# Performance work log

Hardware: AMD Instinct MI355X
Metric: run time of the kernel (lower is better)

The kernel has to match this reference:

```python
import jax, jax.numpy as jnp
import numpy as np

WINDOW = 5
MAX_LEVELS = 4
EPS = 1e-6

_SX = (jnp.array([[-1., 0., 1.], [-2., 0., 2.], [-1., 0., 1.]], dtype=jnp.float32) / 8.0).reshape(1, 1, 3, 3)
_SY = jnp.transpose(_SX, (0, 1, 3, 2))
_DN = ('NCHW', 'OIHW', 'NCHW')


def _avg_pool2(x):
    B, C, H, W = x.shape
    return x.reshape(B, C, H // 2, 2, W // 2, 2).mean(axis=(3, 5))


def _warp(img, flow):
    # bilinear grid_sample, align_corners=True, zeros padding; sample at pixel coords grid+flow
    B, C, H, W = img.shape
    ys, xs = jnp.meshgrid(jnp.arange(H, dtype=img.dtype), jnp.arange(W, dtype=img.dtype), indexing='ij')
    x = xs[None] + flow[:, 0]  # [B,H,W]
    y = ys[None] + flow[:, 1]
    x0f, y0f = jnp.floor(x), jnp.floor(y)
    wx, wy = x - x0f, y - y0f
    imf = img.reshape(B, C, H * W)

    def gather(yi, xi):
        valid = (xi >= 0) & (xi <= W - 1) & (yi >= 0) & (yi <= H - 1)
        xi_c = jnp.clip(xi, 0, W - 1).astype(jnp.int32)
        yi_c = jnp.clip(yi, 0, H - 1).astype(jnp.int32)
        flat = (yi_c * W + xi_c).reshape(B, 1, H * W)
        v = jnp.take_along_axis(imf, jnp.broadcast_to(flat, (B, C, H * W)), axis=2).reshape(B, C, H, W)
        return v * valid[:, None].astype(img.dtype)

    out = (gather(y0f, x0f) * ((1 - wx) * (1 - wy))[:, None]
           + gather(y0f, x0f + 1) * (wx * (1 - wy))[:, None]
           + gather(y0f + 1, x0f) * ((1 - wx) * wy)[:, None]
           + gather(y0f + 1, x0f + 1) * (wx * wy)[:, None])
    return out


def _resize_ac(x, Hn, Wn):
    # bilinear resize, align_corners=True (static shapes)
    B, C, H, W = x.shape
    if (H, W) == (Hn, Wn):
        return x
    ys = jnp.linspace(0.0, H - 1, Hn, dtype=x.dtype)
    xs = jnp.linspace(0.0, W - 1, Wn, dtype=x.dtype)
    y0 = jnp.clip(jnp.floor(ys), 0, H - 2).astype(jnp.int32)
    x0 = jnp.clip(jnp.floor(xs), 0, W - 2).astype(jnp.int32)
    wy = (ys - y0)[None, None, :, None]
    wx = (xs - x0)[None, None, None, :]
    rows = x[:, :, y0, :] * (1 - wy) + x[:, :, y0 + 1, :] * wy
    return rows[:, :, :, x0] * (1 - wx) + rows[:, :, :, x0 + 1] * wx


def _lucas_kanade(I1, I2):
    if I1.shape[1] > 1:
        I1 = I1.mean(1, keepdims=True)
        I2 = I2.mean(1, keepdims=True)
    Ix = jax.lax.conv_general_dilated(I1, _SX, (1, 1), [(1, 1), (1, 1)], dimension_numbers=_DN)
    Iy = jax.lax.conv_general_dilated(I1, _SY, (1, 1), [(1, 1), (1, 1)], dimension_numbers=_DN)
    It = I2 - I1
    # stack all 5 structure-tensor products and box-filter them with one grouped conv
    stats = jnp.concatenate([Ix * Ix, Iy * Iy, Ix * Iy, Ix * It, Iy * It], axis=1)  # [B,5,H,W]
    boxk = jnp.ones((5, 1, WINDOW, WINDOW), dtype=I1.dtype)
    p0 = WINDOW // 2
    p1 = WINDOW - p0 - 1
    S = jax.lax.conv_general_dilated(stats, boxk, (1, 1), [(p0, p1), (p0, p1)],
                                     feature_group_count=5, dimension_numbers=_DN)
    Sxx, Syy, Sxy, Sxt, Syt = jnp.split(S, 5, axis=1)
    inv = 1.0 / (Sxx * Syy - Sxy * Sxy + EPS)
    u = (-Syy * Sxt + Sxy * Syt) * inv
    v = (Sxy * Sxt - Sxx * Syt) * inv
    return jnp.concatenate([u, v], axis=1)


def setup_inputs() -> dict:
    key = jax.random.key(0)
    k1, k2 = jax.random.split(key)
    img1 = jax.random.uniform(k1, (8, 3, 512, 512), dtype=jnp.float32)
    img2 = jax.random.uniform(k2, (8, 3, 512, 512), dtype=jnp.float32)
    return {"img1": img1, "img2": img2}


def reference(img1, img2):
    B, C, H, W = img1.shape
    levels = max(1, MAX_LEVELS)
    pyr1, pyr2 = [img1], [img2]
    for _ in range(1, levels):
        pyr1.append(_avg_pool2(pyr1[-1]))
        pyr2.append(_avg_pool2(pyr2[-1]))
    flow = jnp.zeros((B, 2, pyr1[-1].shape[2], pyr1[-1].shape[3]), dtype=img1.dtype)
    for lvl in range(levels - 1, -1, -1):
        I1, I2 = pyr1[lvl], pyr2[lvl]
        if lvl < levels - 1:
            flow = _resize_ac(flow, I1.shape[2], I1.shape[3]) * 2.0
        I2w = _warp(I2, flow)
        flow = flow + _lucas_kanade(I1, I2w)
    if flow.shape[2:] != (H, W):
        fh, fw = flow.shape[2], flow.shape[3]
        flow = _resize_ac(flow, H, W)
        flow = flow * jnp.array([W / fw, H / fh], dtype=flow.dtype).reshape(1, 2, 1, 1)
    return flow
```

## Files before the change

### kernel.cpp

```cpp
#include <hip/hip_runtime.h>

#define NB 8
#define TS 16
#define PR 20
#define GR 22
#define SW 24

typedef float f2 __attribute__((ext_vector_type(2)));

__global__ void gray_pool_kernel(const float* __restrict__ img1, const float* __restrict__ img2,
                                 float* __restrict__ g0a, float* __restrict__ g0b,
                                 float* __restrict__ g1a, float* __restrict__ g1b) {
    const int W = 512, HW = 512 * 512, Wq = 256, HWq = 256 * 256;
    int i = blockIdx.x * blockDim.x + threadIdx.x;
    if (i >= NB * HWq) return;
    int qx = i % Wq;
    int qy = (i / Wq) % Wq;
    int b = i / HWq;
    size_t base = (size_t)b * 3 * HW + (size_t)(2 * qy) * W + 2 * qx;
    const float third = 1.0f / 3.0f;

    f2 a0c0 = __builtin_nontemporal_load((const f2*)(img1 + base));
    f2 a1c0 = __builtin_nontemporal_load((const f2*)(img1 + base + W));
    f2 a0c1 = __builtin_nontemporal_load((const f2*)(img1 + base + HW));
    f2 a1c1 = __builtin_nontemporal_load((const f2*)(img1 + base + HW + W));
    f2 a0c2 = __builtin_nontemporal_load((const f2*)(img1 + base + 2 * HW));
    f2 a1c2 = __builtin_nontemporal_load((const f2*)(img1 + base + 2 * HW + W));
    float p00 = (a0c0.x + a0c1.x + a0c2.x) * third;
    float p01 = (a0c0.y + a0c1.y + a0c2.y) * third;
    float p10 = (a1c0.x + a1c1.x + a1c2.x) * third;
    float p11 = (a1c0.y + a1c1.y + a1c2.y) * third;
    size_t gbase = (size_t)b * HW + (size_t)(2 * qy) * W + 2 * qx;
    *(f2*)(g0a + gbase) = (f2){p00, p01};
    *(f2*)(g0a + gbase + W) = (f2){p10, p11};
    g1a[(size_t)b * HWq + qy * Wq + qx] = (p00 + p01 + p10 + p11) * 0.25f;

    f2 b0c0 = __builtin_nontemporal_load((const f2*)(img2 + base));
    f2 b1c0 = __builtin_nontemporal_load((const f2*)(img2 + base + W));
    f2 b0c1 = __builtin_nontemporal_load((const f2*)(img2 + base + HW));
    f2 b1c1 = __builtin_nontemporal_load((const f2*)(img2 + base + HW + W));
    f2 b0c2 = __builtin_nontemporal_load((const f2*)(img2 + base + 2 * HW));
    f2 b1c2 = __builtin_nontemporal_load((const f2*)(img2 + base + 2 * HW + W));
    float q00 = (b0c0.x + b0c1.x + b0c2.x) * third;
    float q01 = (b0c0.y + b0c1.y + b0c2.y) * third;
    float q10 = (b1c0.x + b1c1.x + b1c2.x) * third;
    float q11 = (b1c0.y + b1c1.y + b1c2.y) * third;
    *(f2*)(g0b + gbase) = (f2){q00, q01};
    *(f2*)(g0b + gbase + W) = (f2){q10, q11};
    g1b[(size_t)b * HWq + qy * Wq + qx] = (q00 + q01 + q10 + q11) * 0.25f;
}

__global__ void down2_kernel(const float* __restrict__ l1a, const float* __restrict__ l1b,
                             float* __restrict__ l2a, float* __restrict__ l2b,
                             float* __restrict__ l3a, float* __restrict__ l3b) {
    const int W3 = 64, W2 = 128, W1 = 256;
    int i = blockIdx.x * blockDim.x + threadIdx.x;
    int total = 2 * NB * W3 * W3;
    if (i >= total) return;
    int x3 = i % W3;
    int y3 = (i / W3) % W3;
    int b = (i / (W3 * W3)) % NB;
    int j = i / (NB * W3 * W3);
    const float* l1 = (j ? l1b : l1a) + (size_t)b * W1 * W1;
    float* l2 = (j ? l2b : l2a) + (size_t)b * W2 * W2;
    float* l3 = (j ? l3b : l3a) + (size_t)b * W3 * W3;
    float4 r0 = *(const float4*)(l1 + (size_t)(4 * y3 + 0) * W1 + 4 * x3);
    float4 r1 = *(const float4*)(l1 + (size_t)(4 * y3 + 1) * W1 + 4 * x3);
    float4 r2 = *(const float4*)(l1 + (size_t)(4 * y3 + 2) * W1 + 4 * x3);
    float4 r3 = *(const float4*)(l1 + (size_t)(4 * y3 + 3) * W1 + 4 * x3);
    float a00 = (r0.x + r0.y + r1.x + r1.y) * 0.25f;
    float a01 = (r0.z + r0.w + r1.z + r1.w) * 0.25f;
    float a10 = (r2.x + r2.y + r3.x + r3.y) * 0.25f;
    float a11 = (r2.z + r2.w + r3.z + r3.w) * 0.25f;
    *(f2*)(l2 + (size_t)(2 * y3) * W2 + 2 * x3) = (f2){a00, a01};
    *(f2*)(l2 + (size_t)(2 * y3 + 1) * W2 + 2 * x3) = (f2){a10, a11};
    l3[y3 * W3 + x3] = (a00 + a01 + a10 + a11) * 0.25f;
}

template <int MODE>
__global__ __launch_bounds__(256) void lk_kernel(
    const float* __restrict__ g1, const float* __restrict__ g2,
    const float* __restrict__ fin, float* __restrict__ fout, int H, int W) {
    __shared__ float sG[GR][SW];
    __shared__ float sU[PR][SW], sV[PR][SW];
    __shared__ float sP[5][PR][SW];
    __shared__ float sH[5][PR][16];

    int nbx = W / TS;
    int b = blockIdx.x % NB;
    int t = blockIdx.x / NB;
    int ty0 = (t / nbx) * TS, tx0 = (t % nbx) * TS;
    int tid = threadIdx.x;
    int lx = tid % TS, ly = tid / TS;

    const float* G1 = g1 + (size_t)b * H * W;
    const float* G2 = g2 + (size_t)b * H * W;
    bool interior = (ty0 >= 3) && (ty0 + TS + 3 <= H) && (tx0 >= 3) && (tx0 + TS + 3 <= W);

    if (interior) {
        for (int i = tid; i < GR * GR; i += 256) {
            int r = i / GR, c = i % GR;
            sG[r][c] = G1[(ty0 - 3 + r) * W + (tx0 - 3 + c)];
        }
    } else {
        for (int i = tid; i < GR * GR; i += 256) {
            int r = i / GR, c = i % GR;
            int gy = ty0 - 3 + r, gx = tx0 - 3 + c;
            float v = 0.0f;
            if (gy >= 0 && gy < H && gx >= 0 && gx < W) v = G1[gy * W + gx];
            sG[r][c] = v;
        }
    }
    if (MODE == 1) {
        int Hs = H >> 1, Ws = W >> 1;
        float scale = (float)(Hs - 1) / (float)(H - 1);
        const float* FU = fin + (size_t)b * 2 * Hs * Ws;
        const float* FV = FU + Hs * Ws;
        for (int i = tid; i < PR * PR; i += 256) {
            int r = i / PR, c = i % PR;
            int gy = ty0 - 2 + r, gx = tx0 - 2 + c;
            float sy = (float)gy * scale;
            float sx = (float)gx * scale;
            int y0 = min(max((int)sy, 0), Hs - 2);
            int x0 = min(max((int)sx, 0), Ws - 2);
            float wy = sy - (float)y0, wx = sx - (float)x0;
            const float* pu = FU + (size_t)y0 * Ws + x0;
            const float* pv = FV + (size_t)y0 * Ws + x0;
            float ut = pu[0] * (1.0f - wy) + pu[Ws] * wy;
            float ub = pu[1] * (1.0f - wy) + pu[Ws + 1] * wy;
            float vt = pv[0] * (1.0f - wy) + pv[Ws] * wy;
            float vb = pv[1] * (1.0f - wy) + pv[Ws + 1] * wy;
            sU[r][c] = 2.0f * (ut * (1.0f - wx) + ub * wx);
            sV[r][c] = 2.0f * (vt * (1.0f - wx) + vb * wx);
        }
    } else {
        for (int i = tid; i < PR * PR; i += 256) {
            int r = i / PR, c = i % PR;
            sU[r][c] = 0.0f;
            sV[r][c] = 0.0f;
        }
    }
    __syncthreads();

#pragma unroll
    for (int it = 0; it < 2; ++it) {
        int i = tid + it * 256;
        if (i < PR * PR) {
            int r = i / PR, c = i % PR;
            int gy = ty0 - 2 + r, gx = tx0 - 2 + c;
            float su = sU[r][c], sv = sV[r][c];
            float xx = (float)gx + su, yy = (float)gy + sv;
            float x0f = floorf(xx), y0f = floorf(yy);
            float wx = xx - x0f, wy = yy - y0f;
            int xi = (int)x0f, yi = (int)y0f;
            int xc0 = min(max(xi, 0), W - 1), xc1 = min(max(xi + 1, 0), W - 1);
            int yc0 = min(max(yi, 0), H - 1), yc1 = min(max(yi + 1, 0), H - 1);
            float v00 = G2[yc0 * W + xc0];
            float v01 = G2[yc0 * W + xc1];
            float v10 = G2[yc1 * W + xc0];
            float v11 = G2[yc1 * W + xc1];
            float Wm1 = (float)(W - 1), Hm1 = (float)(H - 1);
            float mx0 = (x0f >= 0.0f && x0f <= Wm1) ? 1.0f : 0.0f;
            float mx1 = (x0f + 1.0f >= 0.0f && x0f + 1.0f <= Wm1) ? 1.0f : 0.0f;
            float my0 = (y0f >= 0.0f && y0f <= Hm1) ? 1.0f : 0.0f;
            float my1 = (y0f + 1.0f >= 0.0f && y0f + 1.0f <= Hm1) ? 1.0f : 0.0f;
            float Ix = (-sG[r][c] + sG[r][c + 2]
                        - 2.0f * sG[r + 1][c] + 2.0f * sG[r + 1][c + 2]
                        - sG[r + 2][c] + sG[r + 2][c + 2]) * 0.125f;
            float Iy = (-sG[r][c] - 2.0f * sG[r][c + 1] - sG[r][c + 2]
                        + sG[r + 2][c] + 2.0f * sG[r + 2][c + 1] + sG[r + 2][c + 2]) * 0.125f;
            float I2w = v00 * ((1.0f - wx) * (1.0f - wy) * mx0 * my0)
                      + v01 * (wx * (1.0f - wy) * mx1 * my0)
                      + v10 * ((1.0f - wx) * wy * mx0 * my1)
                      + v11 * (wx * wy * mx1 * my1);
            float It = I2w - sG[r + 1][c + 1];
            float vm = (interior || (gy >= 0 && gy < H && gx >= 0 && gx < W)) ? 1.0f : 0.0f;
            Ix *= vm; Iy *= vm; It *= vm;
            sP[0][r][c] = Ix * Ix;
            sP[1][r][c] = Iy * Iy;
            sP[2][r][c] = Ix * Iy;
            sP[3][r][c] = Ix * It;
            sP[4][r][c] = Iy * It;
        }
    }
    __syncthreads();

    for (int i = tid; i < 5 * PR * 16; i += 256) {
        int x = i % 16;
        int tt = i / 16;
        int r = tt % PR;
        int ch = tt / PR;
        const float* row = &sP[ch][r][x];
        sH[ch][r][x] = row[0] + row[1] + row[2] + row[3] + row[4];
    }
    __syncthreads();

    float Sxx = 0.f, Syy = 0.f, Sxy = 0.f, Sxt = 0.f, Syt = 0.f;
#pragma unroll
    for (int dy = 0; dy < 5; ++dy) {
        Sxx += sH[0][ly + dy][lx];
        Syy += sH[1][ly + dy][lx];
        Sxy += sH[2][ly + dy][lx];
        Sxt += sH[3][ly + dy][lx];
        Syt += sH[4][ly + dy][lx];
    }
    float inv = 1.0f / (Sxx * Syy - Sxy * Sxy + 1e-6f);
    float du = (-Syy * Sxt + Sxy * Syt) * inv;
    float dv = (Sxy * Sxt - Sxx * Syt) * inv;
    int gy = ty0 + ly, gx = tx0 + lx;
    float* FOU = fout + (size_t)b * 2 * H * W;
    FOU[gy * W + gx] = sU[ly + 2][lx + 2] + du;
    FOU[H * W + gy * W + gx] = sV[ly + 2][lx + 2] + dv;
}

extern "C" void kernel_launch(void* const* d_in, const int* in_sizes, int n_in,
                              void* d_out, int out_size, void* d_ws, size_t ws_size,
                              hipStream_t stream) {
    const float* img1 = (const float*)d_in[0];
    const float* img2 = (const float*)d_in[1];
    float* out = (float*)d_out;
    float* ws = (float*)d_ws;

    const int Hl[4] = {512, 256, 128, 64};
    size_t goff[4];
    size_t tot = 0;
    for (int l = 0; l < 4; ++l) {
        goff[l] = tot;
        tot += (size_t)NB * Hl[l] * Hl[l];
    }
    float* p1 = ws;
    float* p2 = ws + tot;
    float* f64 = p2 + tot;
    float* f128 = f64 + (size_t)NB * 2 * 64 * 64;
    float* f256 = f128 + (size_t)NB * 2 * 128 * 128;

    {
        int n = NB * 256 * 256;
        gray_pool_kernel<<<(n + 255) / 256, 256, 0, stream>>>(
            img1, img2, p1 + goff[0], p2 + goff[0], p1 + goff[1], p2 + goff[1]);
    }
    {
        int n = 2 * NB * 64 * 64;
        down2_kernel<<<(n + 255) / 256, 256, 0, stream>>>(
            p1 + goff[1], p2 + goff[1], p1 + goff[2], p2 + goff[2], p1 + goff[3], p2 + goff[3]);
    }
    {
        int nb = NB * (64 / TS) * (64 / TS);
        lk_kernel<0><<<nb, 256, 0, stream>>>(p1 + goff[3], p2 + goff[3], nullptr, f64, 64, 64);
    }
    {
        int nb = NB * (128 / TS) * (128 / TS);
        lk_kernel<1><<<nb, 256, 0, stream>>>(p1 + goff[2], p2 + goff[2], f64, f128, 128, 128);
    }
    {
        int nb = NB * (256 / TS) * (256 / TS);
        lk_kernel<1><<<nb, 256, 0, stream>>>(p1 + goff[1], p2 + goff[1], f128, f256, 256, 256);
    }
    {
        int nb = NB * (512 / TS) * (512 / TS);
        lk_kernel<1><<<nb, 256, 0, stream>>>(p1 + goff[0], p2 + goff[0], f256, out, 512, 512);
    }
}
```

Baseline: 70.85 us.

## Fuse pyramid downsampling with coarsest LK level and stage flow in LDS

Merges the downsample kernel and the 64x64 Lucas-Kanade level into one kernel. Each block rebuilds its 128 and 64 pyramid tiles with halo in shared memory and computes flow directly, which removes one launch and a global round trip. The finer LK levels now stage a small coarse-flow patch in shared memory and upsample from it, instead of gathering from global memory. The upsample is also fused into the warp loop, which drops one barrier. The final level uses nontemporal stores. The cost is redundant halo computation in the fused kernel and only 128 blocks doing the 256-to-128 downsampling work.

```diff
diff --git a/kernel.cpp b/kernel.cpp
--- a/kernel.cpp
+++ b/kernel.cpp
@@ -5,6 +5,7 @@
 #define PR 20
 #define GR 22
 #define SW 24
+#define SFW 12
 
 typedef float f2 __attribute__((ext_vector_type(2)));
 
@@ -50,34 +51,107 @@
     g1b[(size_t)b * HWq + qy * Wq + qx] = (q00 + q01 + q10 + q11) * 0.25f;
 }
 
-__global__ void down2_kernel(const float* __restrict__ l1a, const float* __restrict__ l1b,
-                             float* __restrict__ l2a, float* __restrict__ l2b,
-                             float* __restrict__ l3a, float* __restrict__ l3b) {
-    const int W3 = 64, W2 = 128, W1 = 256;
-    int i = blockIdx.x * blockDim.x + threadIdx.x;
-    int total = 2 * NB * W3 * W3;
-    if (i >= total) return;
-    int x3 = i % W3;
-    int y3 = (i / W3) % W3;
-    int b = (i / (W3 * W3)) % NB;
-    int j = i / (NB * W3 * W3);
-    const float* l1 = (j ? l1b : l1a) + (size_t)b * W1 * W1;
-    float* l2 = (j ? l2b : l2a) + (size_t)b * W2 * W2;
-    float* l3 = (j ? l3b : l3a) + (size_t)b * W3 * W3;
-    float4 r0 = *(const float4*)(l1 + (size_t)(4 * y3 + 0) * W1 + 4 * x3);
-    float4 r1 = *(const float4*)(l1 + (size_t)(4 * y3 + 1) * W1 + 4 * x3);
-    float4 r2 = *(const float4*)(l1 + (size_t)(4 * y3 + 2) * W1 + 4 * x3);
-    float4 r3 = *(const float4*)(l1 + (size_t)(4 * y3 + 3) * W1 + 4 * x3);
-    float a00 = (r0.x + r0.y + r1.x + r1.y) * 0.25f;
-    float a01 = (r0.z + r0.w + r1.z + r1.w) * 0.25f;
-    float a10 = (r2.x + r2.y + r3.x + r3.y) * 0.25f;
-    float a11 = (r2.z + r2.w + r3.z + r3.w) * 0.25f;
-    *(f2*)(l2 + (size_t)(2 * y3) * W2 + 2 * x3) = (f2){a00, a01};
-    *(f2*)(l2 + (size_t)(2 * y3 + 1) * W2 + 2 * x3) = (f2){a10, a11};
-    l3[y3 * W3 + x3] = (a00 + a01 + a10 + a11) * 0.25f;
+__global__ __launch_bounds__(256) void down2_lk64_kernel(
+    const float* __restrict__ l1a, const float* __restrict__ l1b,
+    float* __restrict__ l2a, float* __restrict__ l2b,
+    float* __restrict__ l3a, float* __restrict__ l3b,
+    float* __restrict__ f64) {
+    const int W1 = 256, W2 = 128, W3 = 64;
+    __shared__ float sL2[2][44][45];
+    __shared__ float sG3[2][GR][SW];
+    __shared__ float sP[5][PR][SW];
+    __shared__ float sH[5][PR][16];
+
+    int b = blockIdx.x % NB;
+    int t = blockIdx.x / NB;
+    int ty0 = (t / 4) * TS, tx0 = (t % 4) * TS;
+    int tid = threadIdx.x;
+    int lx = tid % TS, ly = tid / TS;
+
+    for (int i = tid; i < 2 * 44 * 44; i += 256) {
+        int j = i / 1936;
+        int rem = i % 1936;
+        int r = rem / 44, c = rem % 44;
+        int y2 = 2 * ty0 - 6 + r, x2 = 2 * tx0 - 6 + c;
+        float v = 0.0f;
+        if (y2 >= 0 && y2 < W2 && x2 >= 0 && x2 < W2) {
+            const float* l1 = (j ? l1b : l1a) + (size_t)b * W1 * W1;
+            f2 t0 = *(const f2*)(l1 + (size_t)(2 * y2) * W1 + 2 * x2);
+            f2 t1 = *(const f2*)(l1 + (size_t)(2 * y2 + 1) * W1 + 2 * x2);
+            v = (t0.x + t0.y + t1.x + t1.y) * 0.25f;
+            if (r >= 6 && r < 38 && c >= 6 && c < 38)
+                (j ? l2b : l2a)[(size_t)b * W2 * W2 + y2 * W2 + x2] = v;
+        }
+        sL2[j][r][c] = v;
+    }
+    __syncthreads();
+
+    for (int i = tid; i < 2 * GR * GR; i += 256) {
+        int j = i / (GR * GR);
+        int rem = i % (GR * GR);
+        int r = rem / GR, c = rem % GR;
+        float v = (sL2[j][2 * r][2 * c] + sL2[j][2 * r][2 * c + 1]
+                 + sL2[j][2 * r + 1][2 * c] + sL2[j][2 * r + 1][2 * c + 1]) * 0.25f;
+        sG3[j][r][c] = v;
+        if (r >= 3 && r < 19 && c >= 3 && c < 19) {
+            int y3 = ty0 - 3 + r, x3 = tx0 - 3 + c;
+            (j ? l3b : l3a)[(size_t)b * W3 * W3 + y3 * W3 + x3] = v;
+        }
+    }
+    __syncthreads();
+
+#pragma unroll
+    for (int it = 0; it < 2; ++it) {
+        int i = tid + it * 256;
+        if (i < PR * PR) {
+            int r = i / PR, c = i % PR;
+            int gy = ty0 - 2 + r, gx = tx0 - 2 + c;
+            float Ix = (-sG3[0][r][c] + sG3[0][r][c + 2]
+                        - 2.0f * sG3[0][r + 1][c] + 2.0f * sG3[0][r + 1][c + 2]
+                        - sG3[0][r + 2][c] + sG3[0][r + 2][c + 2]) * 0.125f;
+            float Iy = (-sG3[0][r][c] - 2.0f * sG3[0][r][c + 1] - sG3[0][r][c + 2]
+                        + sG3[0][r + 2][c] + 2.0f * sG3[0][r + 2][c + 1] + sG3[0][r + 2][c + 2]) * 0.125f;
+            float It = sG3[1][r + 1][c + 1] - sG3[0][r + 1][c + 1];
+            float vm = (gy >= 0 && gy < W3 && gx >= 0 && gx < W3) ? 1.0f : 0.0f;
+            Ix *= vm; Iy *= vm; It *= vm;
+            sP[0][r][c] = Ix * Ix;
+            sP[1][r][c] = Iy * Iy;
+            sP[2][r][c] = Ix * Iy;
+            sP[3][r][c] = Ix * It;
+            sP[4][r][c] = Iy * It;
+        }
+    }
+    __syncthreads();
+
+    for (int i = tid; i < 5 * PR * 16; i += 256) {
+        int x = i % 16;
+        int tt = i / 16;
+        int r = tt % PR;
+        int ch = tt / PR;
+        const float* row = &sP[ch][r][x];
+        sH[ch][r][x] = row[0] + row[1] + row[2] + row[3] + row[4];
+    }
+    __syncthreads();
+
+    float Sxx = 0.f, Syy = 0.f, Sxy = 0.f, Sxt = 0.f, Syt = 0.f;
+#pragma unroll
+    for (int dy = 0; dy < 5; ++dy) {
+        Sxx += sH[0][ly + dy][lx];
+        Syy += sH[1][ly + dy][lx];
+        Sxy += sH[2][ly + dy][lx];
+        Sxt += sH[3][ly + dy][lx];
+        Syt += sH[4][ly + dy][lx];
+    }
+    float inv = 1.0f / (Sxx * Syy - Sxy * Sxy + 1e-6f);
+    float du = (-Syy * Sxt + Sxy * Syt) * inv;
+    float dv = (Sxy * Sxt - Sxx * Syt) * inv;
+    int gy = ty0 + ly, gx = tx0 + lx;
+    float* FOU = f64 + (size_t)b * 2 * W3 * W3;
+    FOU[gy * W3 + gx] = du;
+    FOU[W3 * W3 + gy * W3 + gx] = dv;
 }
 
-template <int MODE>
+template <int FINAL>
 __global__ __launch_bounds__(256) void lk_kernel(
     const float* __restrict__ g1, const float* __restrict__ g2,
     const float* __restrict__ fin, float* __restrict__ fout, int H, int W) {
@@ -85,6 +159,7 @@
     __shared__ float sU[PR][SW], sV[PR][SW];
     __shared__ float sP[5][PR][SW];
     __shared__ float sH[5][PR][16];
+    __shared__ float sFU[SFW][SFW + 1], sFV[SFW][SFW + 1];
 
     int nbx = W / TS;
     int b = blockIdx.x % NB;
@@ -96,6 +171,13 @@
     const float* G1 = g1 + (size_t)b * H * W;
     const float* G2 = g2 + (size_t)b * H * W;
     bool interior = (ty0 >= 3) && (ty0 + TS + 3 <= H) && (tx0 >= 3) && (tx0 + TS + 3 <= W);
+
+    int Hs = H >> 1, Ws = W >> 1;
+    float scale = (float)(Hs - 1) / (float)(H - 1);
+    int yA = min(max((int)((float)max(ty0 - 2, 0) * scale), 0), Hs - 2);
+    int xA = min(max((int)((float)max(tx0 - 2, 0) * scale), 0), Ws - 2);
+    const float* FU = fin + (size_t)b * 2 * Hs * Ws;
+    const float* FV = FU + Hs * Ws;
 
     if (interior) {
         for (int i = tid; i < GR * GR; i += 256) {
@@ -111,44 +193,37 @@
             sG[r][c] = v;
         }
     }
-    if (MODE == 1) {
-        int Hs = H >> 1, Ws = W >> 1;
-        float scale = (float)(Hs - 1) / (float)(H - 1);
-        const float* FU = fin + (size_t)b * 2 * Hs * Ws;
-        const float* FV = FU + Hs * Ws;
-        for (int i = tid; i < PR * PR; i += 256) {
+    for (int i = tid; i < 2 * SFW * SFW; i += 256) {
+        int ch = i / (SFW * SFW);
+        int rem = i % (SFW * SFW);
+        int r = rem / SFW, c = rem % SFW;
+        int ys = min(yA + r, Hs - 1), xs = min(xA + c, Ws - 1);
+        float v = (ch ? FV : FU)[(size_t)ys * Ws + xs];
+        if (ch) sFV[r][c] = v; else sFU[r][c] = v;
+    }
+    __syncthreads();
+
+#pragma unroll
+    for (int it = 0; it < 2; ++it) {
+        int i = tid + it * 256;
+        if (i < PR * PR) {
             int r = i / PR, c = i % PR;
             int gy = ty0 - 2 + r, gx = tx0 - 2 + c;
             float sy = (float)gy * scale;
             float sx = (float)gx * scale;
             int y0 = min(max((int)sy, 0), Hs - 2);
             int x0 = min(max((int)sx, 0), Ws - 2);
-            float wy = sy - (float)y0, wx = sx - (float)x0;
-            const float* pu = FU + (size_t)y0 * Ws + x0;
-            const float* pv = FV + (size_t)y0 * Ws + x0;
-            float ut = pu[0] * (1.0f - wy) + pu[Ws] * wy;
-            float ub = pu[1] * (1.0f - wy) + pu[Ws + 1] * wy;
-            float vt = pv[0] * (1.0f - wy) + pv[Ws] * wy;
-            float vb = pv[1] * (1.0f - wy) + pv[Ws + 1] * wy;
-            sU[r][c] = 2.0f * (ut * (1.0f - wx) + ub * wx);
-            sV[r][c] = 2.0f * (vt * (1.0f - wx) + vb * wx);
-        }
-    } else {
-        for (int i = tid; i < PR * PR; i += 256) {
-            int r = i / PR, c = i % PR;
-            sU[r][c] = 0.0f;
-            sV[r][c] = 0.0f;
-        }
-    }
-    __syncthreads();
-
-#pragma unroll
-    for (int it = 0; it < 2; ++it) {
-        int i = tid + it * 256;
-        if (i < PR * PR) {
-            int r = i / PR, c = i % PR;
-            int gy = ty0 - 2 + r, gx = tx0 - 2 + c;
-            float su = sU[r][c], sv = sV[r][c];
+            float wyf = sy - (float)y0, wxf = sx - (float)x0;
+            int ry = y0 - yA, rx = x0 - xA;
+            float ut = sFU[ry][rx] * (1.0f - wyf) + sFU[ry + 1][rx] * wyf;
+            float ub = sFU[ry][rx + 1] * (1.0f - wyf) + sFU[ry + 1][rx + 1] * wyf;
+            float vt = sFV[ry][rx] * (1.0f - wyf) + sFV[ry + 1][rx] * wyf;
+            float vb = sFV[ry][rx + 1] * (1.0f - wyf) + sFV[ry + 1][rx + 1] * wyf;
+            float su = 2.0f * (ut * (1.0f - wxf) + ub * wxf);
+            float sv = 2.0f * (vt * (1.0f - wxf) + vb * wxf);
+            sU[r][c] = su;
+            sV[r][c] = sv;
+
             float xx = (float)gx + su, yy = (float)gy + sv;
             float x0f = floorf(xx), y0f = floorf(yy);
             float wx = xx - x0f, wy = yy - y0f;
@@ -209,8 +284,15 @@
     float dv = (Sxy * Sxt - Sxx * Syt) * inv;
     int gy = ty0 + ly, gx = tx0 + lx;
     float* FOU = fout + (size_t)b * 2 * H * W;
-    FOU[gy * W + gx] = sU[ly + 2][lx + 2] + du;
-    FOU[H * W + gy * W + gx] = sV[ly + 2][lx + 2] + dv;
+    float ou = sU[ly + 2][lx + 2] + du;
+    float ov = sV[ly + 2][lx + 2] + dv;
+    if (FINAL) {
+        __builtin_nontemporal_store(ou, &FOU[gy * W + gx]);
+        __builtin_nontemporal_store(ov, &FOU[H * W + gy * W + gx]);
+    } else {
+        FOU[gy * W + gx] = ou;
+        FOU[H * W + gy * W + gx] = ov;
+    }
 }
 
 extern "C" void kernel_launch(void* const* d_in, const int* in_sizes, int n_in,
@@ -240,21 +322,18 @@
             img1, img2, p1 + goff[0], p2 + goff[0], p1 + goff[1], p2 + goff[1]);
     }
     {
-        int n = 2 * NB * 64 * 64;
-        down2_kernel<<<(n + 255) / 256, 256, 0, stream>>>(
-            p1 + goff[1], p2 + goff[1], p1 + goff[2], p2 + goff[2], p1 + goff[3], p2 + goff[3]);
-    }
-    {
-        int nb = NB * (64 / TS) * (64 / TS);
-        lk_kernel<0><<<nb, 256, 0, stream>>>(p1 + goff[3], p2 + goff[3], nullptr, f64, 64, 64);
+        int nb = NB * 4 * 4;
+        down2_lk64_kernel<<<nb, 256, 0, stream>>>(
+            p1 + goff[1], p2 + goff[1], p1 + goff[2], p2 + goff[2],
+            p1 + goff[3], p2 + goff[3], f64);
     }
     {
         int nb = NB * (128 / TS) * (128 / TS);
-        lk_kernel<1><<<nb, 256, 0, stream>>>(p1 + goff[2], p2 + goff[2], f64, f128, 128, 128);
+        lk_kernel<0><<<nb, 256, 0, stream>>>(p1 + goff[2], p2 + goff[2], f64, f128, 128, 128);
     }
     {
         int nb = NB * (256 / TS) * (256 / TS);
-        lk_kernel<1><<<nb, 256, 0, stream>>>(p1 + goff[1], p2 + goff[1], f128, f256, 256, 256);
+        lk_kernel<0><<<nb, 256, 0, stream>>>(p1 + goff[1], p2 + goff[1], f128, f256, 256, 256);
     }
     {
         int nb = NB * (512 / TS) * (512 / TS);
```

Result: slower. 74.95 us (+5.8%).

## Use 32x32 LK tiles with 512 threads and stage coarse flow in LDS

Applied to the files above, without the earlier changes.

Tiles grow from 16x16 to 32x32 outputs per block with 512 threads, each thread producing two outputs. This shrinks the halo overhead for the gradient, warp and window sums. The coarse flow patch is loaded once into shared memory and upsampled on the fly from LDS, recomputed for both the halo region and the outputs, instead of being gathered from global memory into sU/sV. The cost is more shared memory per block and fewer blocks on the small pyramid levels (only 32 blocks at 64x64), which lowers parallelism there.

```diff
diff --git a/kernel.cpp b/kernel.cpp
--- a/kernel.cpp
+++ b/kernel.cpp
@@ -1,10 +1,13 @@
 #include <hip/hip_runtime.h>
 
 #define NB 8
-#define TS 16
-#define PR 20
-#define GR 22
-#define SW 24
+#define BT 32
+#define PR2 36
+#define GR2 38
+#define SGW 40
+#define SPW 40
+#define SHW 32
+#define SFW2 20
 
 typedef float f2 __attribute__((ext_vector_type(2)));
 
@@ -78,139 +81,154 @@
 }
 
 template <int MODE>
-__global__ __launch_bounds__(256) void lk_kernel(
+__global__ __launch_bounds__(512) void lk32_kernel(
     const float* __restrict__ g1, const float* __restrict__ g2,
     const float* __restrict__ fin, float* __restrict__ fout, int H, int W) {
-    __shared__ float sG[GR][SW];
-    __shared__ float sU[PR][SW], sV[PR][SW];
-    __shared__ float sP[5][PR][SW];
-    __shared__ float sH[5][PR][16];
-
-    int nbx = W / TS;
+    __shared__ float sG[GR2][SGW];
+    __shared__ float sP[5][PR2][SPW];
+    __shared__ float sH[5][PR2][SHW];
+    __shared__ float sFU[SFW2][SFW2 + 1], sFV[SFW2][SFW2 + 1];
+
+    int nbx = W / BT;
     int b = blockIdx.x % NB;
     int t = blockIdx.x / NB;
-    int ty0 = (t / nbx) * TS, tx0 = (t % nbx) * TS;
+    int ty0 = (t / nbx) * BT, tx0 = (t % nbx) * BT;
     int tid = threadIdx.x;
-    int lx = tid % TS, ly = tid / TS;
+    int lx = tid % 32, ly = tid / 32;
 
     const float* G1 = g1 + (size_t)b * H * W;
     const float* G2 = g2 + (size_t)b * H * W;
-    bool interior = (ty0 >= 3) && (ty0 + TS + 3 <= H) && (tx0 >= 3) && (tx0 + TS + 3 <= W);
-
+    bool interior = (ty0 >= 3) && (ty0 + BT + 3 <= H) && (tx0 >= 3) && (tx0 + BT + 3 <= W);
+
+    int Hs = H >> 1, Ws = W >> 1;
+    float scale = (float)(Hs - 1) / (float)(H - 1);
+    int yA = 0, xA = 0;
+    if (MODE == 1) {
+        yA = min(max((int)((float)max(ty0 - 2, 0) * scale), 0), Hs - 2);
+        xA = min(max((int)((float)max(tx0 - 2, 0) * scale), 0), Ws - 2);
+        const float* FU = fin + (size_t)b * 2 * Hs * Ws;
+        const float* FV = FU + Hs * Ws;
+        for (int i = tid; i < 2 * SFW2 * SFW2; i += 512) {
+            int ch = i / (SFW2 * SFW2);
+            int rem = i % (SFW2 * SFW2);
+            int r = rem / SFW2, c = rem % SFW2;
+            int ys = min(yA + r, Hs - 1), xs = min(xA + c, Ws - 1);
+            float v = (ch ? FV : FU)[(size_t)ys * Ws + xs];
+            if (ch) sFV[r][c] = v; else sFU[r][c] = v;
+        }
+    }
     if (interior) {
-        for (int i = tid; i < GR * GR; i += 256) {
-            int r = i / GR, c = i % GR;
+        for (int i = tid; i < GR2 * GR2; i += 512) {
+            int r = i / GR2, c = i % GR2;
             sG[r][c] = G1[(ty0 - 3 + r) * W + (tx0 - 3 + c)];
         }
     } else {
-        for (int i = tid; i < GR * GR; i += 256) {
-            int r = i / GR, c = i % GR;
+        for (int i = tid; i < GR2 * GR2; i += 512) {
+            int r = i / GR2, c = i % GR2;
             int gy = ty0 - 3 + r, gx = tx0 - 3 + c;
             float v = 0.0f;
             if (gy >= 0 && gy < H && gx >= 0 && gx < W) v = G1[gy * W + gx];
             sG[r][c] = v;
         }
     }
-    if (MODE == 1) {
-        int Hs = H >> 1, Ws = W >> 1;
-        float scale = (float)(Hs - 1) / (float)(H - 1);
-        const float* FU = fin + (size_t)b * 2 * Hs * Ws;
-        const float* FV = FU + Hs * Ws;
-        for (int i = tid; i < PR * PR; i += 256) {
-            int r = i / PR, c = i % PR;
-            int gy = ty0 - 2 + r, gx = tx0 - 2 + c;
-            float sy = (float)gy * scale;
-            float sx = (float)gx * scale;
+    __syncthreads();
+
+    for (int i = tid; i < PR2 * PR2; i += 512) {
+        int r = i / PR2, c = i % PR2;
+        int gy = ty0 - 2 + r, gx = tx0 - 2 + c;
+        float su = 0.0f, sv = 0.0f;
+        if (MODE == 1) {
+            float sy = (float)gy * scale, sx = (float)gx * scale;
             int y0 = min(max((int)sy, 0), Hs - 2);
             int x0 = min(max((int)sx, 0), Ws - 2);
-            float wy = sy - (float)y0, wx = sx - (float)x0;
-            const float* pu = FU + (size_t)y0 * Ws + x0;
-            const float* pv = FV + (size_t)y0 * Ws + x0;
-            float ut = pu[0] * (1.0f - wy) + pu[Ws] * wy;
-            float ub = pu[1] * (1.0f - wy) + pu[Ws + 1] * wy;
-            float vt = pv[0] * (1.0f - wy) + pv[Ws] * wy;
-            float vb = pv[1] * (1.0f - wy) + pv[Ws + 1] * wy;
-            sU[r][c] = 2.0f * (ut * (1.0f - wx) + ub * wx);
-            sV[r][c] = 2.0f * (vt * (1.0f - wx) + vb * wx);
-        }
-    } else {
-        for (int i = tid; i < PR * PR; i += 256) {
-            int r = i / PR, c = i % PR;
-            sU[r][c] = 0.0f;
-            sV[r][c] = 0.0f;
-        }
+            float wyf = sy - (float)y0, wxf = sx - (float)x0;
+            int ry = y0 - yA, rx = x0 - xA;
+            float ut = sFU[ry][rx] * (1.0f - wyf) + sFU[ry + 1][rx] * wyf;
+            float ub = sFU[ry][rx + 1] * (1.0f - wyf) + sFU[ry + 1][rx + 1] * wyf;
+            float vt = sFV[ry][rx] * (1.0f - wyf) + sFV[ry + 1][rx] * wyf;
+            float vb = sFV[ry][rx + 1] * (1.0f - wyf) + sFV[ry + 1][rx + 1] * wyf;
+            su = 2.0f * (ut * (1.0f - wxf) + ub * wxf);
+            sv = 2.0f * (vt * (1.0f - wxf) + vb * wxf);
+        }
+        float xx = (float)gx + su, yy = (float)gy + sv;
+        float x0f = floorf(xx), y0f = floorf(yy);
+        float wx = xx - x0f, wy = yy - y0f;
+        int xi = (int)x0f, yi = (int)y0f;
+        int xc0 = min(max(xi, 0), W - 1), xc1 = min(max(xi + 1, 0), W - 1);
+        int yc0 = min(max(yi, 0), H - 1), yc1 = min(max(yi + 1, 0), H - 1);
+        float v00 = G2[yc0 * W + xc0];
+        float v01 = G2[yc0 * W + xc1];
+        float v10 = G2[yc1 * W + xc0];
+        float v11 = G2[yc1 * W + xc1];
+        float Wm1 = (float)(W - 1), Hm1 = (float)(H - 1);
+        float mx0 = (x0f >= 0.0f && x0f <= Wm1) ? 1.0f : 0.0f;
+        float mx1 = (x0f + 1.0f >= 0.0f && x0f + 1.0f <= Wm1) ? 1.0f : 0.0f;
+        float my0 = (y0f >= 0.0f && y0f <= Hm1) ? 1.0f : 0.0f;
+        float my1 = (y0f + 1.0f >= 0.0f && y0f + 1.0f <= Hm1) ? 1.0f : 0.0f;
+        float Ix = (-sG[r][c] + sG[r][c + 2]
+                    - 2.0f * sG[r + 1][c] + 2.0f * sG[r + 1][c + 2]
+                    - sG[r + 2][c] + sG[r + 2][c + 2]) * 0.125f;
+        float Iy = (-sG[r][c] - 2.0f * sG[r][c + 1] - sG[r][c + 2]
+                    + sG[r + 2][c] + 2.0f * sG[r + 2][c + 1] + sG[r + 2][c + 2]) * 0.125f;
+        float I2w = v00 * ((1.0f - wx) * (1.0f - wy) * mx0 * my0)
+                  + v01 * (wx * (1.0f - wy) * mx1 * my0)
+                  + v10 * ((1.0f - wx) * wy * mx0 * my1)
+                  + v11 * (wx * wy * mx1 * my1);
+        float It = I2w - sG[r + 1][c + 1];
+        float vm = (interior || (gy >= 0 && gy < H && gx >= 0 && gx < W)) ? 1.0f : 0.0f;
+        Ix *= vm; Iy *= vm; It *= vm;
+        sP[0][r][c] = Ix * Ix;
+        sP[1][r][c] = Iy * Iy;
+        sP[2][r][c] = Ix * Iy;
+        sP[3][r][c] = Ix * It;
+        sP[4][r][c] = Iy * It;
     }
     __syncthreads();
 
-#pragma unroll
-    for (int it = 0; it < 2; ++it) {
-        int i = tid + it * 256;
-        if (i < PR * PR) {
-            int r = i / PR, c = i % PR;
-            int gy = ty0 - 2 + r, gx = tx0 - 2 + c;
-            float su = sU[r][c], sv = sV[r][c];
-            float xx = (float)gx + su, yy = (float)gy + sv;
-            float x0f = floorf(xx), y0f = floorf(yy);
-            float wx = xx - x0f, wy = yy - y0f;
-            int xi = (int)x0f, yi = (int)y0f;
-            int xc0 = min(max(xi, 0), W - 1), xc1 = min(max(xi + 1, 0), W - 1);
-            int yc0 = min(max(yi, 0), H - 1), yc1 = min(max(yi + 1, 0), H - 1);
-            float v00 = G2[yc0 * W + xc0];
-            float v01 = G2[yc0 * W + xc1];
-            float v10 = G2[yc1 * W + xc0];
-            float v11 = G2[yc1 * W + xc1];
-            float Wm1 = (float)(W - 1), Hm1 = (float)(H - 1);
-            float mx0 = (x0f >= 0.0f && x0f <= Wm1) ? 1.0f : 0.0f;
-            float mx1 = (x0f + 1.0f >= 0.0f && x0f + 1.0f <= Wm1) ? 1.0f : 0.0f;
-            float my0 = (y0f >= 0.0f && y0f <= Hm1) ? 1.0f : 0.0f;
-            float my1 = (y0f + 1.0f >= 0.0f && y0f + 1.0f <= Hm1) ? 1.0f : 0.0f;
-            float Ix = (-sG[r][c] + sG[r][c + 2]
-                        - 2.0f * sG[r + 1][c] + 2.0f * sG[r + 1][c + 2]
-                        - sG[r + 2][c] + sG[r + 2][c + 2]) * 0.125f;
-            float Iy = (-sG[r][c] - 2.0f * sG[r][c + 1] - sG[r][c + 2]
-                        + sG[r + 2][c] + 2.0f * sG[r + 2][c + 1] + sG[r + 2][c + 2]) * 0.125f;
-            float I2w = v00 * ((1.0f - wx) * (1.0f - wy) * mx0 * my0)
-                      + v01 * (wx * (1.0f - wy) * mx1 * my0)
-                      + v10 * ((1.0f - wx) * wy * mx0 * my1)
-                      + v11 * (wx * wy * mx1 * my1);
-            float It = I2w - sG[r + 1][c + 1];
-            float vm = (interior || (gy >= 0 && gy < H && gx >= 0 && gx < W)) ? 1.0f : 0.0f;
-            Ix *= vm; Iy *= vm; It *= vm;
-            sP[0][r][c] = Ix * Ix;
-            sP[1][r][c] = Iy * Iy;
-            sP[2][r][c] = Ix * Iy;
-            sP[3][r][c] = Ix * It;
-            sP[4][r][c] = Iy * It;
-        }
-    }
-    __syncthreads();
-
-    for (int i = tid; i < 5 * PR * 16; i += 256) {
-        int x = i % 16;
-        int tt = i / 16;
-        int r = tt % PR;
-        int ch = tt / PR;
+    for (int i = tid; i < 5 * PR2 * 32; i += 512) {
+        int x = i % 32;
+        int tt = i / 32;
+        int r = tt % PR2;
+        int ch = tt / PR2;
         const float* row = &sP[ch][r][x];
         sH[ch][r][x] = row[0] + row[1] + row[2] + row[3] + row[4];
     }
     __syncthreads();
 
-    float Sxx = 0.f, Syy = 0.f, Sxy = 0.f, Sxt = 0.f, Syt = 0.f;
+    float* FOU = fout + (size_t)b * 2 * H * W;
 #pragma unroll
-    for (int dy = 0; dy < 5; ++dy) {
-        Sxx += sH[0][ly + dy][lx];
-        Syy += sH[1][ly + dy][lx];
-        Sxy += sH[2][ly + dy][lx];
-        Sxt += sH[3][ly + dy][lx];
-        Syt += sH[4][ly + dy][lx];
-    }
-    float inv = 1.0f / (Sxx * Syy - Sxy * Sxy + 1e-6f);
-    float du = (-Syy * Sxt + Sxy * Syt) * inv;
-    float dv = (Sxy * Sxt - Sxx * Syt) * inv;
-    int gy = ty0 + ly, gx = tx0 + lx;
-    float* FOU = fout + (size_t)b * 2 * H * W;
-    FOU[gy * W + gx] = sU[ly + 2][lx + 2] + du;
-    FOU[H * W + gy * W + gx] = sV[ly + 2][lx + 2] + dv;
+    for (int k = 0; k < 2; ++k) {
+        int oly = ly + k * 16;
+        float Sxx = 0.f, Syy = 0.f, Sxy = 0.f, Sxt = 0.f, Syt = 0.f;
+#pragma unroll
+        for (int dy = 0; dy < 5; ++dy) {
+            Sxx += sH[0][oly + dy][lx];
+            Syy += sH[1][oly + dy][lx];
+            Sxy += sH[2][oly + dy][lx];
+            Sxt += sH[3][oly + dy][lx];
+            Syt += sH[4][oly + dy][lx];
+        }
+        float inv = 1.0f / (Sxx * Syy - Sxy * Sxy + 1e-6f);
+        float du = (-Syy * Sxt + Sxy * Syt) * inv;
+        float dv = (Sxy * Sxt - Sxx * Syt) * inv;
+        int gy = ty0 + oly, gx = tx0 + lx;
+        float su = 0.0f, sv = 0.0f;
+        if (MODE == 1) {
+            float sy = (float)gy * scale, sx = (float)gx * scale;
+            int y0 = min(max((int)sy, 0), Hs - 2);
+            int x0 = min(max((int)sx, 0), Ws - 2);
+            float wyf = sy - (float)y0, wxf = sx - (float)x0;
+            int ry = y0 - yA, rx = x0 - xA;
+            float ut = sFU[ry][rx] * (1.0f - wyf) + sFU[ry + 1][rx] * wyf;
+            float ub = sFU[ry][rx + 1] * (1.0f - wyf) + sFU[ry + 1][rx + 1] * wyf;
+            float vt = sFV[ry][rx] * (1.0f - wyf) + sFV[ry + 1][rx] * wyf;
+            float vb = sFV[ry][rx + 1] * (1.0f - wyf) + sFV[ry + 1][rx + 1] * wyf;
+            su = 2.0f * (ut * (1.0f - wxf) + ub * wxf);
+            sv = 2.0f * (vt * (1.0f - wxf) + vb * wxf);
+        }
+        FOU[gy * W + gx] = su + du;
+        FOU[H * W + gy * W + gx] = sv + dv;
+    }
 }
 
 extern "C" void kernel_launch(void* const* d_in, const int* in_sizes, int n_in,
@@ -245,19 +263,19 @@
             p1 + goff[1], p2 + goff[1], p1 + goff[2], p2 + goff[2], p1 + goff[3], p2 + goff[3]);
     }
     {
-        int nb = NB * (64 / TS) * (64 / TS);
-        lk_kernel<0><<<nb, 256, 0, stream>>>(p1 + goff[3], p2 + goff[3], nullptr, f64, 64, 64);
-    }
-    {
-        int nb = NB * (128 / TS) * (128 / TS);
-        lk_kernel<1><<<nb, 256, 0, stream>>>(p1 + goff[2], p2 + goff[2], f64, f128, 128, 128);
-    }
-    {
-        int nb = NB * (256 / TS) * (256 / TS);
-        lk_kernel<1><<<nb, 256, 0, stream>>>(p1 + goff[1], p2 + goff[1], f128, f256, 256, 256);
-    }
-    {
-        int nb = NB * (512 / TS) * (512 / TS);
-        lk_kernel<1><<<nb, 256, 0, stream>>>(p1 + goff[0], p2 + goff[0], f256, out, 512, 512);
-    }
-}
+        int nb = NB * (64 / BT) * (64 / BT);
+        lk32_kernel<0><<<nb, 512, 0, stream>>>(p1 + goff[3], p2 + goff[3], nullptr, f64, 64, 64);
+    }
+    {
+        int nb = NB * (128 / BT) * (128 / BT);
+        lk32_kernel<1><<<nb, 512, 0, stream>>>(p1 + goff[2], p2 + goff[2], f64, f128, 128, 128);
+    }
+    {
+        int nb = NB * (256 / BT) * (256 / BT);
+        lk32_kernel<1><<<nb, 512, 0, stream>>>(p1 + goff[1], p2 + goff[1], f128, f256, 256, 256);
+    }
+    {
+        int nb = NB * (512 / BT) * (512 / BT);
+        lk32_kernel<1><<<nb, 512, 0, stream>>>(p1 + goff[0], p2 + goff[0], f256, out, 512, 512);
+    }
+}
```

After: 74.19 us. 4.7% more time.

## Stage warp source window and coarse flow tile in LDS for LK kernel

Applied to the files above, without the earlier changes.

Loads a 28x28 window of the second image into shared memory so bilinear warp samples come from LDS, falling back to global reads only when the displaced sample leaves the window. Also stages a 12x12 patch of the coarse flow in LDS and recomputes the upsampled flow per pixel from it, replacing the per-pixel global gathers and the sU/sV arrays. This trades scattered global loads for extra LDS traffic, a branch, and recomputed interpolation.

```diff
diff --git a/kernel.cpp b/kernel.cpp
--- a/kernel.cpp
+++ b/kernel.cpp
@@ -5,6 +5,9 @@
 #define PR 20
 #define GR 22
 #define SW 24
+#define SFW 12
+#define GW 28
+#define GWS 29
 
 typedef float f2 __attribute__((ext_vector_type(2)));
 
@@ -82,9 +85,10 @@
     const float* __restrict__ g1, const float* __restrict__ g2,
     const float* __restrict__ fin, float* __restrict__ fout, int H, int W) {
     __shared__ float sG[GR][SW];
-    __shared__ float sU[PR][SW], sV[PR][SW];
+    __shared__ float sG2[GW][GWS];
     __shared__ float sP[5][PR][SW];
     __shared__ float sH[5][PR][16];
+    __shared__ float sFU[SFW][SFW + 1], sFV[SFW][SFW + 1];
 
     int nbx = W / TS;
     int b = blockIdx.x % NB;
@@ -97,6 +101,23 @@
     const float* G2 = g2 + (size_t)b * H * W;
     bool interior = (ty0 >= 3) && (ty0 + TS + 3 <= H) && (tx0 >= 3) && (tx0 + TS + 3 <= W);
 
+    int Hs = H >> 1, Ws = W >> 1;
+    float scale = (float)(Hs - 1) / (float)(H - 1);
+    int yA = 0, xA = 0;
+    if (MODE == 1) {
+        yA = min(max((int)((float)max(ty0 - 2, 0) * scale), 0), Hs - 2);
+        xA = min(max((int)((float)max(tx0 - 2, 0) * scale), 0), Ws - 2);
+        const float* FU = fin + (size_t)b * 2 * Hs * Ws;
+        const float* FV = FU + Hs * Ws;
+        for (int i = tid; i < 2 * SFW * SFW; i += 256) {
+            int ch = i / (SFW * SFW);
+            int rem = i % (SFW * SFW);
+            int r = rem / SFW, c = rem % SFW;
+            int ys = min(yA + r, Hs - 1), xs = min(xA + c, Ws - 1);
+            float v = (ch ? FV : FU)[(size_t)ys * Ws + xs];
+            if (ch) sFV[r][c] = v; else sFU[r][c] = v;
+        }
+    }
     if (interior) {
         for (int i = tid; i < GR * GR; i += 256) {
             int r = i / GR, c = i % GR;
@@ -111,33 +132,21 @@
             sG[r][c] = v;
         }
     }
-    if (MODE == 1) {
-        int Hs = H >> 1, Ws = W >> 1;
-        float scale = (float)(Hs - 1) / (float)(H - 1);
-        const float* FU = fin + (size_t)b * 2 * Hs * Ws;
-        const float* FV = FU + Hs * Ws;
-        for (int i = tid; i < PR * PR; i += 256) {
-            int r = i / PR, c = i % PR;
-            int gy = ty0 - 2 + r, gx = tx0 - 2 + c;
-            float sy = (float)gy * scale;
-            float sx = (float)gx * scale;
-            int y0 = min(max((int)sy, 0), Hs - 2);
-            int x0 = min(max((int)sx, 0), Ws - 2);
-            float wy = sy - (float)y0, wx = sx - (float)x0;
-            const float* pu = FU + (size_t)y0 * Ws + x0;
-            const float* pv = FV + (size_t)y0 * Ws + x0;
-            float ut = pu[0] * (1.0f - wy) + pu[Ws] * wy;
-            float ub = pu[1] * (1.0f - wy) + pu[Ws + 1] * wy;
-            float vt = pv[0] * (1.0f - wy) + pv[Ws] * wy;
-            float vb = pv[1] * (1.0f - wy) + pv[Ws + 1] * wy;
-            sU[r][c] = 2.0f * (ut * (1.0f - wx) + ub * wx);
-            sV[r][c] = 2.0f * (vt * (1.0f - wx) + vb * wx);
-        }
-    } else {
-        for (int i = tid; i < PR * PR; i += 256) {
-            int r = i / PR, c = i % PR;
-            sU[r][c] = 0.0f;
-            sV[r][c] = 0.0f;
+    {
+        bool winin = (ty0 >= 5) && (ty0 + 23 <= H) && (tx0 >= 5) && (tx0 + 23 <= W);
+        if (winin) {
+            for (int i = tid; i < GW * GW; i += 256) {
+                int r = i / GW, c = i % GW;
+                sG2[r][c] = G2[(ty0 - 5 + r) * W + (tx0 - 5 + c)];
+            }
+        } else {
+            for (int i = tid; i < GW * GW; i += 256) {
+                int r = i / GW, c = i % GW;
+                int gy = ty0 - 5 + r, gx = tx0 - 5 + c;
+                float v = 0.0f;
+                if (gy >= 0 && gy < H && gx >= 0 && gx < W) v = G2[gy * W + gx];
+                sG2[r][c] = v;
+            }
         }
     }
     __syncthreads();
@@ -148,31 +157,52 @@
         if (i < PR * PR) {
             int r = i / PR, c = i % PR;
             int gy = ty0 - 2 + r, gx = tx0 - 2 + c;
-            float su = sU[r][c], sv = sV[r][c];
+            float su = 0.0f, sv = 0.0f;
+            if (MODE == 1) {
+                float sy = (float)gy * scale, sx = (float)gx * scale;
+                int y0 = min(max((int)sy, 0), Hs - 2);
+                int x0 = min(max((int)sx, 0), Ws - 2);
+                float wyf = sy - (float)y0, wxf = sx - (float)x0;
+                int ry = y0 - yA, rx = x0 - xA;
+                float ut = sFU[ry][rx] * (1.0f - wyf) + sFU[ry + 1][rx] * wyf;
+                float ub = sFU[ry][rx + 1] * (1.0f - wyf) + sFU[ry + 1][rx + 1] * wyf;
+                float vt = sFV[ry][rx] * (1.0f - wyf) + sFV[ry + 1][rx] * wyf;
+                float vb = sFV[ry][rx + 1] * (1.0f - wyf) + sFV[ry + 1][rx + 1] * wyf;
+                su = 2.0f * (ut * (1.0f - wxf) + ub * wxf);
+                sv = 2.0f * (vt * (1.0f - wxf) + vb * wxf);
+            }
             float xx = (float)gx + su, yy = (float)gy + sv;
             float x0f = floorf(xx), y0f = floorf(yy);
             float wx = xx - x0f, wy = yy - y0f;
-            int xi = (int)x0f, yi = (int)y0f;
-            int xc0 = min(max(xi, 0), W - 1), xc1 = min(max(xi + 1, 0), W - 1);
-            int yc0 = min(max(yi, 0), H - 1), yc1 = min(max(yi + 1, 0), H - 1);
-            float v00 = G2[yc0 * W + xc0];
-            float v01 = G2[yc0 * W + xc1];
-            float v10 = G2[yc1 * W + xc0];
-            float v11 = G2[yc1 * W + xc1];
             float Wm1 = (float)(W - 1), Hm1 = (float)(H - 1);
             float mx0 = (x0f >= 0.0f && x0f <= Wm1) ? 1.0f : 0.0f;
             float mx1 = (x0f + 1.0f >= 0.0f && x0f + 1.0f <= Wm1) ? 1.0f : 0.0f;
             float my0 = (y0f >= 0.0f && y0f <= Hm1) ? 1.0f : 0.0f;
             float my1 = (y0f + 1.0f >= 0.0f && y0f + 1.0f <= Hm1) ? 1.0f : 0.0f;
+            float w00 = (1.0f - wx) * (1.0f - wy) * mx0 * my0;
+            float w01 = wx * (1.0f - wy) * mx1 * my0;
+            float w10 = (1.0f - wx) * wy * mx0 * my1;
+            float w11 = wx * wy * mx1 * my1;
+            bool inwin = (y0f >= (float)(ty0 - 5)) && (y0f <= (float)(ty0 + 21))
+                      && (x0f >= (float)(tx0 - 5)) && (x0f <= (float)(tx0 + 21));
+            float I2w;
+            if (__builtin_expect(inwin, 1)) {
+                int ry = (int)y0f - (ty0 - 5);
+                int rx = (int)x0f - (tx0 - 5);
+                I2w = sG2[ry][rx] * w00 + sG2[ry][rx + 1] * w01
+                    + sG2[ry + 1][rx] * w10 + sG2[ry + 1][rx + 1] * w11;
+            } else {
+                int xi = (int)x0f, yi = (int)y0f;
+                int xc0 = min(max(xi, 0), W - 1), xc1 = min(max(xi + 1, 0), W - 1);
+                int yc0 = min(max(yi, 0), H - 1), yc1 = min(max(yi + 1, 0), H - 1);
+                I2w = G2[yc0 * W + xc0] * w00 + G2[yc0 * W + xc1] * w01
+                    + G2[yc1 * W + xc0] * w10 + G2[yc1 * W + xc1] * w11;
+            }
             float Ix = (-sG[r][c] + sG[r][c + 2]
                         - 2.0f * sG[r + 1][c] + 2.0f * sG[r + 1][c + 2]
                         - sG[r + 2][c] + sG[r + 2][c + 2]) * 0.125f;
             float Iy = (-sG[r][c] - 2.0f * sG[r][c + 1] - sG[r][c + 2]
                         + sG[r + 2][c] + 2.0f * sG[r + 2][c + 1] + sG[r + 2][c + 2]) * 0.125f;
-            float I2w = v00 * ((1.0f - wx) * (1.0f - wy) * mx0 * my0)
-                      + v01 * (wx * (1.0f - wy) * mx1 * my0)
-                      + v10 * ((1.0f - wx) * wy * mx0 * my1)
-                      + v11 * (wx * wy * mx1 * my1);
             float It = I2w - sG[r + 1][c + 1];
             float vm = (interior || (gy >= 0 && gy < H && gx >= 0 && gx < W)) ? 1.0f : 0.0f;
             Ix *= vm; Iy *= vm; It *= vm;
@@ -208,9 +238,23 @@
     float du = (-Syy * Sxt + Sxy * Syt) * inv;
     float dv = (Sxy * Sxt - Sxx * Syt) * inv;
     int gy = ty0 + ly, gx = tx0 + lx;
+    float su = 0.0f, sv = 0.0f;
+    if (MODE == 1) {
+        float sy = (float)gy * scale, sx = (float)gx * scale;
+        int y0 = min(max((int)sy, 0), Hs - 2);
+        int x0 = min(max((int)sx, 0), Ws - 2);
+        float wyf = sy - (float)y0, wxf = sx - (float)x0;
+        int ry = y0 - yA, rx = x0 - xA;
+        float ut = sFU[ry][rx] * (1.0f - wyf) + sFU[ry + 1][rx] * wyf;
+        float ub = sFU[ry][rx + 1] * (1.0f - wyf) + sFU[ry + 1][rx + 1] * wyf;
+        float vt = sFV[ry][rx] * (1.0f - wyf) + sFV[ry + 1][rx] * wyf;
+        float vb = sFV[ry][rx + 1] * (1.0f - wyf) + sFV[ry + 1][rx + 1] * wyf;
+        su = 2.0f * (ut * (1.0f - wxf) + ub * wxf);
+        sv = 2.0f * (vt * (1.0f - wxf) + vb * wxf);
+    }
     float* FOU = fout + (size_t)b * 2 * H * W;
-    FOU[gy * W + gx] = sU[ly + 2][lx + 2] + du;
-    FOU[H * W + gy * W + gx] = sV[ly + 2][lx + 2] + dv;
+    FOU[gy * W + gx] = su + du;
+    FOU[H * W + gy * W + gx] = sv + dv;
 }
 
 extern "C" void kernel_launch(void* const* d_in, const int* in_sizes, int n_in,
```

New measurement: 79.94 us. +12.8%, slower.
